# Optimization experiments

Hardware: AMD Instinct MI355X
Metric: run time of the kernel (lower is better)

Reference implementation:

```python
import jax, jax.numpy as jnp
import numpy as np
import math

E = 1024   # embedding_size
H = 16     # layer_size (num heads)
DK = 64    # key_size
DH = 64    # head_size
HID = 4096 # hidden_size
B = 2
S = 2048   # context_size
EPS = 1e-5


def layer_norm(x, w, b):
    mu = jnp.mean(x, axis=-1, keepdims=True)
    var = jnp.mean(jnp.square(x - mu), axis=-1, keepdims=True)
    return (x - mu) * jax.lax.rsqrt(var + EPS) * w + b


def setup_inputs() -> dict:
    key = jax.random.key(0)
    ks = jax.random.split(key, 16)
    sE = 1.0 / math.sqrt(E)
    sH = 1.0 / math.sqrt(HID)
    return {
        "embeddings": jax.random.normal(ks[0], (B, S, E), dtype=jnp.float32),
        "Wq": jax.random.uniform(ks[1], (H, E, DK), minval=-sE, maxval=sE, dtype=jnp.float32),
        "bq": jnp.zeros((H, DK), dtype=jnp.float32),
        "Wk": jax.random.uniform(ks[2], (H, E, DK), minval=-sE, maxval=sE, dtype=jnp.float32),
        "bk": jnp.zeros((H, DK), dtype=jnp.float32),
        "Wv": jax.random.uniform(ks[3], (H, E, DH), minval=-sE, maxval=sE, dtype=jnp.float32),
        "bv": jnp.zeros((H, DH), dtype=jnp.float32),
        "ln1_w": jnp.ones((E,), dtype=jnp.float32),
        "ln1_b": jnp.zeros((E,), dtype=jnp.float32),
        "ln2_w": jnp.ones((E,), dtype=jnp.float32),
        "ln2_b": jnp.zeros((E,), dtype=jnp.float32),
        "W1": jax.random.uniform(ks[4], (E, HID), minval=-sE, maxval=sE, dtype=jnp.float32),
        "b1": jnp.zeros((HID,), dtype=jnp.float32),
        "W2": jax.random.uniform(ks[5], (HID, E), minval=-sH, maxval=sH, dtype=jnp.float32),
        "b2": jnp.zeros((E,), dtype=jnp.float32),
    }


def reference(embeddings, Wq, bq, Wk, bk, Wv, bv, ln1_w, ln1_b, ln2_w, ln2_b, W1, b1, W2, b2):
    # NOTE: faithful to source: residual uses the POST-norm activations
    # (embeddings is reassigned to the LayerNorm output before the residual add).
    x = layer_norm(embeddings, ln1_w, ln1_b)            # [B,S,E]
    q = jnp.einsum('bse,hed->bhsd', x, Wq) + bq[:, None, :]
    k = jnp.einsum('bse,hed->bhsd', x, Wk) + bk[:, None, :]
    v = jnp.einsum('bse,hed->bhsd', x, Wv) + bv[:, None, :]
    scores = jnp.einsum('bhsd,bhtd->bhst', q, k) / math.sqrt(DK)  # [B,H,S,S]
    causal = jnp.tril(jnp.ones((S, S), dtype=bool))
    scores = jnp.where(causal, scores, -jnp.inf)
    w = jax.nn.softmax(scores, axis=-1)
    o = jnp.einsum('bhst,bhtd->bhsd', w, v)             # [B,H,S,DH]
    o = jnp.transpose(o, (0, 2, 1, 3)).reshape(B, S, H * DH)  # concat heads
    x = x + o
    y = layer_norm(x, ln2_w, ln2_b)
    h = jax.nn.relu(jnp.einsum('bse,eh->bsh', y, W1) + b1)
    out = y + jnp.einsum('bsh,he->bse', h, W2) + b2
    return out
```

## Files before the change

kernel.cpp:

```cpp
#include <hip/hip_runtime.h>


typedef unsigned short u16;
typedef unsigned int   u32;
typedef __bf16 bf16x8 __attribute__((ext_vector_type(8)));
typedef float  f32x4  __attribute__((ext_vector_type(4)));

#define NEG_INF (-__builtin_inff())

#if __has_builtin(__builtin_amdgcn_exp2f)
#define EXP2F(x) __builtin_amdgcn_exp2f(x)
#else
#define EXP2F(x) exp2f(x)
#endif

__device__ __forceinline__ u32 pack_bf16_trunc(float a, float b) {
#if __has_builtin(__builtin_amdgcn_perm)
  return __builtin_amdgcn_perm(__float_as_uint(b), __float_as_uint(a), 0x07060302u);
#else
  return (__float_as_uint(a) >> 16) | (__float_as_uint(b) & 0xFFFF0000u);
#endif
}

__device__ __forceinline__ u16 f2b(float f) {
  u32 u = __float_as_uint(f);
  u = (u + 0x7fffu + ((u >> 16) & 1u)) >> 16;
  return (u16)u;
}

__device__ __forceinline__ void gload16(const void* g, void* l) {
  __builtin_amdgcn_global_load_lds(
      (const __attribute__((address_space(1))) u32*)g,
      (__attribute__((address_space(3))) u32*)l, 16, 0, 0);
}

__device__ __forceinline__ bf16x8 ld16(const u16* p) { return *(const bf16x8*)p; }

__device__ __forceinline__
void ln_body(int row, const float* __restrict__ in, const float* __restrict__ in2,
             const float* __restrict__ w, const float* __restrict__ b,
             float* __restrict__ outf, u16* __restrict__ outb) {
  int t = threadIdx.x;
  const float4* ip = (const float4*)(in + (size_t)row * 1024);
  float4 x = ip[t];
  if (in2) {
    const float4* ip2 = (const float4*)(in2 + (size_t)row * 1024);
    float4 o = ip2[t];
    x.x += o.x; x.y += o.y; x.z += o.z; x.w += o.w;
  }
  float s = x.x + x.y + x.z + x.w;
  float q = x.x * x.x + x.y * x.y + x.z * x.z + x.w * x.w;
#pragma unroll
  for (int m = 32; m; m >>= 1) { s += __shfl_xor(s, m); q += __shfl_xor(q, m); }
  __shared__ float rs[4], rq[4];
  if ((t & 63) == 0) { rs[t >> 6] = s; rq[t >> 6] = q; }
  __syncthreads();
  s = rs[0] + rs[1] + rs[2] + rs[3];
  q = rq[0] + rq[1] + rq[2] + rq[3];
  float mean = s * (1.f / 1024.f);
  float var  = q * (1.f / 1024.f) - mean * mean;
  float rstd = rsqrtf(var + 1e-5f);
  float4 wv = ((const float4*)w)[t];
  float4 bv = ((const float4*)b)[t];
  float4 y;
  y.x = (x.x - mean) * rstd * wv.x + bv.x;
  y.y = (x.y - mean) * rstd * wv.y + bv.y;
  y.z = (x.z - mean) * rstd * wv.z + bv.z;
  y.w = (x.w - mean) * rstd * wv.w + bv.w;
  if (outf) ((float4*)(outf + (size_t)row * 1024))[t] = y;
  ushort4 ub;
  ub.x = f2b(y.x); ub.y = f2b(y.y); ub.z = f2b(y.z); ub.w = f2b(y.w);
  ((ushort4*)(outb + (size_t)row * 1024))[t] = ub;
}

__device__ __forceinline__
void trans_body(float* tile, const float* __restrict__ in, u16* __restrict__ out,
                int R, int C, int r0, int c0) {
  int tr = threadIdx.x >> 6, tc = threadIdx.x & 63;
#pragma unroll
  for (int i = 0; i < 16; i++) {
    int r = i * 4 + tr;
    tile[r * 65 + tc] = in[(size_t)(r0 + r) * C + c0 + tc];
  }
  __syncthreads();
#pragma unroll
  for (int i = 0; i < 16; i++) {
    int c = i * 4 + tr;
    out[(size_t)(c0 + c) * R + r0 + tc] = f2b(tile[tc * 65 + c]);
  }
}

__global__ __launch_bounds__(256)
void prologue_k(const float* __restrict__ emb, const float* __restrict__ ln1w,
                const float* __restrict__ ln1b, float* __restrict__ x,
                u16* __restrict__ xb, const float* __restrict__ Wq,
                const float* __restrict__ Wk, const float* __restrict__ Wv,
                u16* __restrict__ Wqkv_t) {
  __shared__ float tile[64 * 65];
  int bx = blockIdx.x;
  if (bx < 4096) {
    ln_body(bx, emb, nullptr, ln1w, ln1b, x, xb);
  } else {
    int id = bx - 4096;
    int z = id >> 4, sub = z & 15, which = z >> 4;
    const float* in = which == 0 ? Wq : (which == 1 ? Wk : Wv);
    trans_body(tile, in + (size_t)sub * 1024 * 64,
               Wqkv_t + (size_t)which * 1024 * 1024 + (size_t)sub * 64 * 1024,
               1024, 64, (id & 15) * 64, 0);
  }
}

__global__ __launch_bounds__(256)
void vtrans_k(const u16* __restrict__ vin, u16* __restrict__ vt) {
  __shared__ __align__(16) u16 tile[64][72];
  int s0 = blockIdx.x * 64, bh = blockIdx.y;
  const u16* ip = vin + (size_t)bh * 2048 * 64;
  u16* op = vt + (size_t)bh * 64 * 2048;
  int t = threadIdx.x;
#pragma unroll
  for (int i = 0; i < 2; i++) {
    int idx = i * 256 + t, r = idx >> 3, c = idx & 7;
    *(uint4*)&tile[r][c * 8] = *(const uint4*)(ip + (size_t)(s0 + r) * 64 + c * 8);
  }
  __syncthreads();
#pragma unroll
  for (int i = 0; i < 16; i++) {
    int d = i * 4 + (t >> 6), s = t & 63;
    op[(size_t)d * 2048 + s0 + s] = tile[s][d];
  }
}

__global__ __launch_bounds__(256)
void ln_k(const float* __restrict__ in, const float* __restrict__ in2,
          const float* __restrict__ w, const float* __restrict__ b,
          float* __restrict__ outf, u16* __restrict__ outb) {
  ln_body(blockIdx.x, in, in2, w, b, outf, outb);
}

#define EPI_QKV  0
#define EPI_RELU 1
#define EPI_RES  2

#define QSCALE 0.18033688011112042f

template <int EPI>
__device__ __forceinline__
void gemm_body(u16* __restrict__ As, u16* __restrict__ Bs,
               const u16* __restrict__ A, const u16* __restrict__ Bt,
               int bxm, int bxn, int kbeg, int klen, int lda, int ldbt,
               const float* __restrict__ bias0, const float* __restrict__ bias1,
               const float* __restrict__ bias2, const float* __restrict__ res,
               int ldout, u16* __restrict__ outb, float* __restrict__ outf,
               float* __restrict__ p1, float* __restrict__ p2, int z) {
  int t = threadIdx.x;
  int wave = t >> 6, lane = t & 63, quad = lane >> 4, l16 = lane & 15;
  int x7 = l16 & 7;
  int wm = (wave >> 1) * 64, wn = (wave & 1) * 64;
  int bm = bxm * 128, bn = bxn * 128;

  const u16* Agl[4];
  const u16* Bgl[4];
#pragma unroll
  for (int i = 0; i < 4; i++) {
    int idx = i * 256 + t, r = idx >> 3, c = (idx & 7) ^ (r & 7);
    Agl[i] = A + (size_t)(bm + r) * lda + kbeg + c * 8;
    Bgl[i] = Bt + (size_t)(bn + r) * ldbt + kbeg + c * 8;
  }
  u16* Asl = As + t * 8;
  u16* Bsl = Bs + t * 8;

  f32x4 acc[4][4] = {};

  for (int k0 = 0; k0 < klen; k0 += 64) {
#pragma unroll
    for (int i = 0; i < 4; i++) {
      gload16(Agl[i] + k0, Asl + i * 2048);
      gload16(Bgl[i] + k0, Bsl + i * 2048);
    }
    __syncthreads();
#pragma unroll
    for (int kc = 0; kc < 2; kc++) {
      bf16x8 af[4], bfr[4];
#pragma unroll
      for (int i = 0; i < 4; i++) {
        int r = wm + i * 16 + l16;
        af[i] = *(const bf16x8*)(As + r * 64 + (((kc * 4 + quad) ^ x7) * 8));
      }
#pragma unroll
      for (int j = 0; j < 4; j++) {
        int r = wn + j * 16 + l16;
        bfr[j] = *(const bf16x8*)(Bs + r * 64 + (((kc * 4 + quad) ^ x7) * 8));
      }
#pragma unroll
      for (int i = 0; i < 4; i++)
#pragma unroll
        for (int j = 0; j < 4; j++)
          acc[i][j] = __builtin_amdgcn_mfma_f32_16x16x32_bf16(af[i], bfr[j],
                                                              acc[i][j], 0, 0, 0);
    }
    __syncthreads();
  }

#pragma unroll
  for (int i = 0; i < 4; i++) {
#pragma unroll
    for (int j = 0; j < 4; j++) {
      int c = bn + wn + j * 16 + l16;
#pragma unroll
      for (int rr = 0; rr < 4; rr++) {
        int r = bm + wm + i * 16 + quad * 4 + rr;
        float v = acc[i][j][rr];
        if (EPI == EPI_QKV) {
          int which = c >> 10, h = (c >> 6) & 15, d = c & 63;
          const float* bp = which == 0 ? bias0 : (which == 1 ? bias1 : bias2);
          v += bp[h * 64 + d];
          if (which == 0) v *= QSCALE;
          int bb = r >> 11, ss = r & 2047;
          outb[((size_t)(which * 32 + bb * 16 + h) * 2048 + ss) * 64 + d] = f2b(v);
        } else if (EPI == EPI_RELU) {
          v += bias0[c];
          v = v > 0.f ? v : 0.f;
          outb[(size_t)r * ldout + c] = f2b(v);
        } else {
          if (z == 0) {
            v += bias0[c] + res[(size_t)r * ldout + c];
            outf[(size_t)r * ldout + c] = v;
          } else if (z == 1) {
            p1[(size_t)r * ldout + c] = v;
          } else {
            p2[(size_t)r * ldout + c] = v;
          }
        }
      }
    }
  }
}

__global__ __launch_bounds__(256)
void qkv_plus_k(const u16* __restrict__ xb, const u16* __restrict__ Wqkv_t,
                const float* __restrict__ bq, const float* __restrict__ bk,
                const float* __restrict__ bv, u16* __restrict__ qkvb,
                const float* __restrict__ W1, const float* __restrict__ W2,
                u16* __restrict__ W1t, u16* __restrict__ W2t) {
  __shared__ __align__(16) u16 SM[2][128 * 64];
  int bx = blockIdx.x;
  if (bx < 768) {
    gemm_body<EPI_QKV>(SM[0], SM[1], xb, Wqkv_t, bx & 31, bx >> 5, 0, 1024,
                       1024, 1024, bq, bk, bv, nullptr, 0, qkvb, nullptr,
                       nullptr, nullptr, 0);
  } else {
    int id = bx - 768;
    float* tile = (float*)SM;
    if (id < 1024)
      trans_body(tile, W1, W1t, 1024, 4096, (id & 15) * 64, (id >> 4) * 64);
    else {
      id -= 1024;
      trans_body(tile, W2, W2t, 4096, 1024, (id >> 4) * 64, (id & 15) * 64);
    }
  }
}

__global__ __launch_bounds__(256)
void ffn1_gemm(const u16* __restrict__ A, const u16* __restrict__ Bt,
               const float* __restrict__ b0, u16* __restrict__ outb) {
  __shared__ __align__(16) u16 SM[2][128 * 64];
  gemm_body<EPI_RELU>(SM[0], SM[1], A, Bt, blockIdx.x, blockIdx.y, 0, 1024,
                      1024, 1024, b0, nullptr, nullptr, nullptr, 4096, outb,
                      nullptr, nullptr, nullptr, 0);
}

__global__ __launch_bounds__(256)
void ffn2_gemm(const u16* __restrict__ A, const u16* __restrict__ Bt,
               const float* __restrict__ b0, const float* __restrict__ res,
               float* __restrict__ outf, float* __restrict__ p1,
               float* __restrict__ p2) {
  __shared__ __align__(16) u16 SM[2][128 * 64];
  int z = blockIdx.z;
  int kbeg = z * 1344 + (z > 0 ? 64 : 0);
  int klen = 1344 + (z == 0 ? 64 : 0);
  gemm_body<EPI_RES>(SM[0], SM[1], A, Bt, blockIdx.x, blockIdx.y, kbeg, klen,
                     4096, 4096, b0, nullptr, nullptr, res, 1024, nullptr,
                     outf, p1, p2, z);
}

__global__ __launch_bounds__(256)
void reduce2_k(float* __restrict__ out, const float* __restrict__ p1,
               const float* __restrict__ p2) {
  int i = blockIdx.x * 256 + threadIdx.x;
  float4 a = ((const float4*)p1)[i];
  float4 c = ((const float4*)p2)[i];
  float4 b = ((float4*)out)[i];
  b.x += a.x + c.x; b.y += a.y + c.y; b.z += a.z + c.z; b.w += a.w + c.w;
  ((float4*)out)[i] = b;
}

__global__ __launch_bounds__(512, 6)
void attn_k(const u16* __restrict__ qkv, const u16* __restrict__ vt,
            float* __restrict__ o) {
  int bh = blockIdx.y, b = bh >> 4, h = bh & 15;
  int Qt = b ? (15 - (int)blockIdx.x) : (int)blockIdx.x;
  int t = threadIdx.x;
  int wave = t >> 6, lane = t & 63, quad = lane >> 4, l16 = lane & 15;
  int x7 = l16 & 7;
  int q0 = Qt * 128 + wave * 16;

  const u16* qg = qkv + (size_t)bh * (2048 * 64);
  const u16* kg = qkv + (size_t)(32 + bh) * (2048 * 64);
  const u16* vg = vt + (size_t)bh * (64 * 2048);

  __shared__ __align__(16) u16 Ks[2][64 * 64];
  __shared__ __align__(16) u16 Vs[2][64 * 64];
  __shared__ __align__(16) u16 Ps[8][16 * 64 + 32];
  u16* Pw = Ps[wave];
  float* auxf = (float*)(Pw + 1024);

  int sr = t >> 3, sc_ = (t & 7) ^ (sr & 7);

  gload16(kg + (size_t)sr * 64 + sc_ * 8, Ks[0] + t * 8);
  gload16(vg + (size_t)sr * 2048 + sc_ * 8, Vs[0] + t * 8);

  bf16x8 qf0 = ld16(qg + (size_t)(q0 + l16) * 64 + quad * 8);
  bf16x8 qf1 = ld16(qg + (size_t)(q0 + l16) * 64 + 32 + quad * 8);

  f32x4 oacc[4] = {};
  float mo = NEG_INF, ll = 0.f;
  int kmax_w = q0 >> 6;
  int klast = 2 * Qt + 1;

  __syncthreads();

  for (int kt = 0; kt <= klast; kt++) {
    const u16* ks = Ks[kt & 1];
    const u16* vs = Vs[kt & 1];
    if (kt < klast) {
      gload16(kg + (size_t)((kt + 1) * 64 + sr) * 64 + sc_ * 8, Ks[(kt + 1) & 1] + t * 8);
      gload16(vg + (size_t)sr * 2048 + (kt + 1) * 64 + sc_ * 8, Vs[(kt + 1) & 1] + t * 8);
    }
    if (kt <= kmax_w) {
      f32x4 sc[4];
#pragma unroll
      for (int g = 0; g < 4; g++) {
        const u16* kr = ks + (g * 16 + l16) * 64;
        bf16x8 kf0 = *(const bf16x8*)(kr + ((quad ^ x7) * 8));
        bf16x8 kf1 = *(const bf16x8*)(kr + (((4 + quad) ^ x7) * 8));
        f32x4 s = {};
        s = __builtin_amdgcn_mfma_f32_16x16x32_bf16(kf0, qf0, s, 0, 0, 0);
        s = __builtin_amdgcn_mfma_f32_16x16x32_bf16(kf1, qf1, s, 0, 0, 0);
        sc[g] = s;
      }

      if (kt == kmax_w) {
#pragma unroll
        for (int g = 0; g < 4; g++) {
          int kvb = kt * 64 + g * 16 + quad * 4;
#pragma unroll
          for (int rr = 0; rr < 4; rr++)
            if (kvb + rr > q0 + l16) sc[g][rr] = NEG_INF;
        }
      }

      float mx = sc[0][0];
#pragma unroll
      for (int g = 0; g < 4; g++)
#pragma unroll
        for (int rr = 0; rr < 4; rr++) mx = fmaxf(mx, sc[g][rr]);
      mx = fmaxf(mx, __shfl_xor(mx, 16));
      mx = fmaxf(mx, __shfl_xor(mx, 32));
      float mnew = fmaxf(mo, mx);
      float al = EXP2F(mo - mnew);
      mo = mnew;

      float sum = 0.f;
#pragma unroll
      for (int g = 0; g < 4; g++) {
        float p0 = EXP2F(sc[g][0] - mnew);
        float p1 = EXP2F(sc[g][1] - mnew);
        float p2 = EXP2F(sc[g][2] - mnew);
        float p3 = EXP2F(sc[g][3] - mnew);
        sum += (p0 + p1) + (p2 + p3);
        u32 lo = pack_bf16_trunc(p0, p1);
        u32 hi = pack_bf16_trunc(p2, p3);
        int slot = (2 * g + (quad >> 1)) ^ x7;
        *(uint2*)(Pw + l16 * 64 + slot * 8 + (quad & 1) * 4) = make_uint2(lo, hi);
      }
      sum += __shfl_xor(sum, 16);
      sum += __shfl_xor(sum, 32);
      ll = ll * al + sum;

      if (lane < 16) auxf[lane] = al;
      f32x4 av = *(const f32x4*)(auxf + quad * 4);
#pragma unroll
      for (int g = 0; g < 4; g++)
#pragma unroll
        for (int rr = 0; rr < 4; rr++) oacc[g][rr] *= av[rr];

      bf16x8 pf0 = *(const bf16x8*)(Pw + l16 * 64 + ((quad ^ x7) * 8));
      bf16x8 pf1 = *(const bf16x8*)(Pw + l16 * 64 + (((4 + quad) ^ x7) * 8));
#pragma unroll
      for (int g = 0; g < 4; g++) {
        const u16* vr = vs + (g * 16 + l16) * 64;
        bf16x8 vf0 = *(const bf16x8*)(vr + ((quad ^ x7) * 8));
        bf16x8 vf1 = *(const bf16x8*)(vr + (((4 + quad) ^ x7) * 8));
        oacc[g] = __builtin_amdgcn_mfma_f32_16x16x32_bf16(pf0, vf0, oacc[g], 0, 0, 0);
        oacc[g] = __builtin_amdgcn_mfma_f32_16x16x32_bf16(pf1, vf1, oacc[g], 0, 0, 0);
      }
    }
    __syncthreads();
  }

  if (lane < 16) auxf[lane] = ll;
  f32x4 lv = *(const f32x4*)(auxf + quad * 4);
  float rinv[4];
#pragma unroll
  for (int rr = 0; rr < 4; rr++) rinv[rr] = 1.f / lv[rr];
  float* op = o + ((size_t)b * 2048 + q0) * 1024 + h * 64;
#pragma unroll
  for (int g = 0; g < 4; g++)
#pragma unroll
    for (int rr = 0; rr < 4; rr++)
      op[(size_t)(quad * 4 + rr) * 1024 + g * 16 + l16] = oacc[g][rr] * rinv[rr];
}

extern "C" void kernel_launch(void* const* d_in, const int* in_sizes, int n_in,
                              void* d_out, int out_size, void* d_ws, size_t ws_size,
                              hipStream_t stream) {
  const float* emb  = (const float*)d_in[0];
  const float* Wq   = (const float*)d_in[1];
  const float* bq   = (const float*)d_in[2];
  const float* Wk   = (const float*)d_in[3];
  const float* bk   = (const float*)d_in[4];
  const float* Wv   = (const float*)d_in[5];
  const float* bv   = (const float*)d_in[6];
  const float* ln1w = (const float*)d_in[7];
  const float* ln1b = (const float*)d_in[8];
  const float* ln2w = (const float*)d_in[9];
  const float* ln2b = (const float*)d_in[10];
  const float* W1   = (const float*)d_in[11];
  const float* b1   = (const float*)d_in[12];
  const float* W2   = (const float*)d_in[13];
  const float* b2   = (const float*)d_in[14];
  float* out = (float*)d_out;

  char* p = (char*)d_ws;
  u16*   Wqkv_t = (u16*)p;   p += (size_t)3072 * 1024 * 2;
  u16*   W2t    = (u16*)p;   p += (size_t)1024 * 4096 * 2;
  u16*   W1t    = (u16*)p;   p += (size_t)4096 * 1024 * 2;
  float* x      = (float*)p; p += (size_t)4096 * 1024 * 4;
  u16*   xb     = (u16*)p;   p += (size_t)4096 * 1024 * 2;
  u16*   qkvb   = (u16*)p;   p += (size_t)3 * 32 * 2048 * 64 * 2;
  float* ob     = (float*)p; p += (size_t)4096 * 1024 * 4;
  float* y      = (float*)p; p += (size_t)4096 * 1024 * 4;
  u16*   yb     = (u16*)p;   p += (size_t)4096 * 1024 * 2;
  u16*   hb     = (u16*)qkvb;
  u16*   vT     = (u16*)y;
  float* part1  = (float*)W1t;
  float* part2  = (float*)((char*)x + (size_t)4096 * 1024 * 2);
  if (ws_size < (size_t)(p - (char*)d_ws)) return;

  prologue_k<<<dim3(4096 + 768), 256, 0, stream>>>(
      emb, ln1w, ln1b, x, xb, Wq, Wk, Wv, Wqkv_t);

  qkv_plus_k<<<dim3(768 + 2048), 256, 0, stream>>>(
      xb, Wqkv_t, bq, bk, bv, qkvb, W1, W2, W1t, W2t);

  vtrans_k<<<dim3(32, 32), 256, 0, stream>>>(qkvb + (size_t)64 * 2048 * 64, vT);

  attn_k<<<dim3(16, 32), 512, 0, stream>>>(qkvb, vT, ob);

  ln_k<<<dim3(4096), 256, 0, stream>>>(x, ob, ln2w, ln2b, y, yb);

  ffn1_gemm<<<dim3(32, 32), 256, 0, stream>>>(yb, W1t, b1, hb);

  ffn2_gemm<<<dim3(32, 8, 3), 256, 0, stream>>>(hb, W2t, b2, y, out, part1, part2);

  reduce2_k<<<dim3(4096), 256, 0, stream>>>(out, part1, part2);
}
```

Measured before the change: 336.0 us.

## Have each attention wave own two query tiles and cut FFN2 split-K to two

The attention kernel now runs 4 waves of 256 threads instead of 8 waves of 512. Each wave handles two 16-row query groups 64 rows apart, so the K and V fragments read from shared memory are loaded once per tile and reused for both groups. This cuts LDS traffic but raises register pressure, and the launch bounds change to 3 blocks per CU. Separately, the FFN2 split-K drops from three slices to two, which removes one partial buffer and lightens the reduction, at the cost of fewer blocks and longer K loops per block.

```diff
diff --git a/kernel.cpp b/kernel.cpp
--- a/kernel.cpp
+++ b/kernel.cpp
@@ -151,7 +151,7 @@
                const float* __restrict__ bias0, const float* __restrict__ bias1,
                const float* __restrict__ bias2, const float* __restrict__ res,
                int ldout, u16* __restrict__ outb, float* __restrict__ outf,
-               float* __restrict__ p1, float* __restrict__ p2, int z) {
+               float* __restrict__ p1, int z) {
   int t = threadIdx.x;
   int wave = t >> 6, lane = t & 63, quad = lane >> 4, l16 = lane & 15;
   int x7 = l16 & 7;
@@ -225,10 +225,8 @@
           if (z == 0) {
             v += bias0[c] + res[(size_t)r * ldout + c];
             outf[(size_t)r * ldout + c] = v;
-          } else if (z == 1) {
+          } else {
             p1[(size_t)r * ldout + c] = v;
-          } else {
-            p2[(size_t)r * ldout + c] = v;
           }
         }
       }
@@ -247,7 +245,7 @@
   if (bx < 768) {
     gemm_body<EPI_QKV>(SM[0], SM[1], xb, Wqkv_t, bx & 31, bx >> 5, 0, 1024,
                        1024, 1024, bq, bk, bv, nullptr, 0, qkvb, nullptr,
-                       nullptr, nullptr, 0);
+                       nullptr, 0);
   } else {
     int id = bx - 768;
     float* tile = (float*)SM;
@@ -266,35 +264,30 @@
   __shared__ __align__(16) u16 SM[2][128 * 64];
   gemm_body<EPI_RELU>(SM[0], SM[1], A, Bt, blockIdx.x, blockIdx.y, 0, 1024,
                       1024, 1024, b0, nullptr, nullptr, nullptr, 4096, outb,
-                      nullptr, nullptr, nullptr, 0);
+                      nullptr, nullptr, 0);
 }
 
 __global__ __launch_bounds__(256)
 void ffn2_gemm(const u16* __restrict__ A, const u16* __restrict__ Bt,
                const float* __restrict__ b0, const float* __restrict__ res,
-               float* __restrict__ outf, float* __restrict__ p1,
-               float* __restrict__ p2) {
+               float* __restrict__ outf, float* __restrict__ p1) {
   __shared__ __align__(16) u16 SM[2][128 * 64];
   int z = blockIdx.z;
-  int kbeg = z * 1344 + (z > 0 ? 64 : 0);
-  int klen = 1344 + (z == 0 ? 64 : 0);
-  gemm_body<EPI_RES>(SM[0], SM[1], A, Bt, blockIdx.x, blockIdx.y, kbeg, klen,
+  gemm_body<EPI_RES>(SM[0], SM[1], A, Bt, blockIdx.x, blockIdx.y, z * 2048, 2048,
                      4096, 4096, b0, nullptr, nullptr, res, 1024, nullptr,
-                     outf, p1, p2, z);
-}
-
-__global__ __launch_bounds__(256)
-void reduce2_k(float* __restrict__ out, const float* __restrict__ p1,
-               const float* __restrict__ p2) {
+                     outf, p1, z);
+}
+
+__global__ __launch_bounds__(256)
+void reduce_k(float* __restrict__ out, const float* __restrict__ p1) {
   int i = blockIdx.x * 256 + threadIdx.x;
   float4 a = ((const float4*)p1)[i];
-  float4 c = ((const float4*)p2)[i];
   float4 b = ((float4*)out)[i];
-  b.x += a.x + c.x; b.y += a.y + c.y; b.z += a.z + c.z; b.w += a.w + c.w;
+  b.x += a.x; b.y += a.y; b.z += a.z; b.w += a.w;
   ((float4*)out)[i] = b;
 }
 
-__global__ __launch_bounds__(512, 6)
+__global__ __launch_bounds__(256, 3)
 void attn_k(const u16* __restrict__ qkv, const u16* __restrict__ vt,
             float* __restrict__ o) {
   int bh = blockIdx.y, b = bh >> 4, h = bh & 15;
@@ -302,7 +295,7 @@
   int t = threadIdx.x;
   int wave = t >> 6, lane = t & 63, quad = lane >> 4, l16 = lane & 15;
   int x7 = l16 & 7;
-  int q0 = Qt * 128 + wave * 16;
+  int qb = Qt * 128 + wave * 16;
 
   const u16* qg = qkv + (size_t)bh * (2048 * 64);
   const u16* kg = qkv + (size_t)(32 + bh) * (2048 * 64);
@@ -311,20 +304,24 @@
   __shared__ __align__(16) u16 Ks[2][64 * 64];
   __shared__ __align__(16) u16 Vs[2][64 * 64];
   __shared__ __align__(16) u16 Ps[8][16 * 64 + 32];
-  u16* Pw = Ps[wave];
-  float* auxf = (float*)(Pw + 1024);
-
-  int sr = t >> 3, sc_ = (t & 7) ^ (sr & 7);
-
-  gload16(kg + (size_t)sr * 64 + sc_ * 8, Ks[0] + t * 8);
-  gload16(vg + (size_t)sr * 2048 + sc_ * 8, Vs[0] + t * 8);
-
-  bf16x8 qf0 = ld16(qg + (size_t)(q0 + l16) * 64 + quad * 8);
-  bf16x8 qf1 = ld16(qg + (size_t)(q0 + l16) * 64 + 32 + quad * 8);
-
-  f32x4 oacc[4] = {};
-  float mo = NEG_INF, ll = 0.f;
-  int kmax_w = q0 >> 6;
+
+#pragma unroll
+  for (int i = 0; i < 2; i++) {
+    int idx = i * 256 + t, r = idx >> 3, c = (idx & 7) ^ (r & 7);
+    gload16(kg + (size_t)r * 64 + c * 8, Ks[0] + idx * 8);
+    gload16(vg + (size_t)r * 2048 + c * 8, Vs[0] + idx * 8);
+  }
+
+  bf16x8 qf[2][2];
+#pragma unroll
+  for (int G = 0; G < 2; G++) {
+    const u16* qr = qg + (size_t)(qb + G * 64 + l16) * 64;
+    qf[G][0] = ld16(qr + quad * 8);
+    qf[G][1] = ld16(qr + 32 + quad * 8);
+  }
+
+  f32x4 oacc[2][4] = {};
+  float mo[2] = {NEG_INF, NEG_INF}, ll[2] = {0.f, 0.f};
   int klast = 2 * Qt + 1;
 
   __syncthreads();
@@ -333,23 +330,42 @@
     const u16* ks = Ks[kt & 1];
     const u16* vs = Vs[kt & 1];
     if (kt < klast) {
-      gload16(kg + (size_t)((kt + 1) * 64 + sr) * 64 + sc_ * 8, Ks[(kt + 1) & 1] + t * 8);
-      gload16(vg + (size_t)sr * 2048 + (kt + 1) * 64 + sc_ * 8, Vs[(kt + 1) & 1] + t * 8);
-    }
-    if (kt <= kmax_w) {
+#pragma unroll
+      for (int i = 0; i < 2; i++) {
+        int idx = i * 256 + t, r = idx >> 3, c = (idx & 7) ^ (r & 7);
+        gload16(kg + (size_t)((kt + 1) * 64 + r) * 64 + c * 8, Ks[(kt + 1) & 1] + idx * 8);
+        gload16(vg + (size_t)r * 2048 + (kt + 1) * 64 + c * 8, Vs[(kt + 1) & 1] + idx * 8);
+      }
+    }
+
+    bf16x8 kf[4][2], vf[4][2];
+#pragma unroll
+    for (int g = 0; g < 4; g++) {
+      const u16* kr = ks + (g * 16 + l16) * 64;
+      kf[g][0] = *(const bf16x8*)(kr + ((quad ^ x7) * 8));
+      kf[g][1] = *(const bf16x8*)(kr + (((4 + quad) ^ x7) * 8));
+      const u16* vr = vs + (g * 16 + l16) * 64;
+      vf[g][0] = *(const bf16x8*)(vr + ((quad ^ x7) * 8));
+      vf[g][1] = *(const bf16x8*)(vr + (((4 + quad) ^ x7) * 8));
+    }
+
+#pragma unroll
+    for (int G = 0; G < 2; G++) {
+      int kdiag = klast - 1 + G;
+      if (kt > kdiag) continue;
+      int q0 = qb + G * 64;
+      u16* Pw = Ps[wave * 2 + G];
+      float* auxf = (float*)(Pw + 1024);
+
       f32x4 sc[4];
 #pragma unroll
       for (int g = 0; g < 4; g++) {
-        const u16* kr = ks + (g * 16 + l16) * 64;
-        bf16x8 kf0 = *(const bf16x8*)(kr + ((quad ^ x7) * 8));
-        bf16x8 kf1 = *(const bf16x8*)(kr + (((4 + quad) ^ x7) * 8));
         f32x4 s = {};
-        s = __builtin_amdgcn_mfma_f32_16x16x32_bf16(kf0, qf0, s, 0, 0, 0);
-        s = __builtin_amdgcn_mfma_f32_16x16x32_bf16(kf1, qf1, s, 0, 0, 0);
+        s = __builtin_amdgcn_mfma_f32_16x16x32_bf16(kf[g][0], qf[G][0], s, 0, 0, 0);
+        s = __builtin_amdgcn_mfma_f32_16x16x32_bf16(kf[g][1], qf[G][1], s, 0, 0, 0);
         sc[g] = s;
       }
-
-      if (kt == kmax_w) {
+      if (kt == kdiag) {
 #pragma unroll
         for (int g = 0; g < 4; g++) {
           int kvb = kt * 64 + g * 16 + quad * 4;
@@ -366,9 +382,9 @@
         for (int rr = 0; rr < 4; rr++) mx = fmaxf(mx, sc[g][rr]);
       mx = fmaxf(mx, __shfl_xor(mx, 16));
       mx = fmaxf(mx, __shfl_xor(mx, 32));
-      float mnew = fmaxf(mo, mx);
-      float al = EXP2F(mo - mnew);
-      mo = mnew;
+      float mnew = fmaxf(mo[G], mx);
+      float al = EXP2F(mo[G] - mnew);
+      mo[G] = mnew;
 
       float sum = 0.f;
 #pragma unroll
@@ -385,40 +401,42 @@
       }
       sum += __shfl_xor(sum, 16);
       sum += __shfl_xor(sum, 32);
-      ll = ll * al + sum;
+      ll[G] = ll[G] * al + sum;
 
       if (lane < 16) auxf[lane] = al;
       f32x4 av = *(const f32x4*)(auxf + quad * 4);
 #pragma unroll
       for (int g = 0; g < 4; g++)
 #pragma unroll
-        for (int rr = 0; rr < 4; rr++) oacc[g][rr] *= av[rr];
+        for (int rr = 0; rr < 4; rr++) oacc[G][g][rr] *= av[rr];
 
       bf16x8 pf0 = *(const bf16x8*)(Pw + l16 * 64 + ((quad ^ x7) * 8));
       bf16x8 pf1 = *(const bf16x8*)(Pw + l16 * 64 + (((4 + quad) ^ x7) * 8));
 #pragma unroll
       for (int g = 0; g < 4; g++) {
-        const u16* vr = vs + (g * 16 + l16) * 64;
-        bf16x8 vf0 = *(const bf16x8*)(vr + ((quad ^ x7) * 8));
-        bf16x8 vf1 = *(const bf16x8*)(vr + (((4 + quad) ^ x7) * 8));
-        oacc[g] = __builtin_amdgcn_mfma_f32_16x16x32_bf16(pf0, vf0, oacc[g], 0, 0, 0);
-        oacc[g] = __builtin_amdgcn_mfma_f32_16x16x32_bf16(pf1, vf1, oacc[g], 0, 0, 0);
+        oacc[G][g] = __builtin_amdgcn_mfma_f32_16x16x32_bf16(pf0, vf[g][0], oacc[G][g], 0, 0, 0);
+        oacc[G][g] = __builtin_amdgcn_mfma_f32_16x16x32_bf16(pf1, vf[g][1], oacc[G][g], 0, 0, 0);
       }
     }
     __syncthreads();
   }
 
-  if (lane < 16) auxf[lane] = ll;
-  f32x4 lv = *(const f32x4*)(auxf + quad * 4);
-  float rinv[4];
-#pragma unroll
-  for (int rr = 0; rr < 4; rr++) rinv[rr] = 1.f / lv[rr];
-  float* op = o + ((size_t)b * 2048 + q0) * 1024 + h * 64;
-#pragma unroll
-  for (int g = 0; g < 4; g++)
-#pragma unroll
-    for (int rr = 0; rr < 4; rr++)
-      op[(size_t)(quad * 4 + rr) * 1024 + g * 16 + l16] = oacc[g][rr] * rinv[rr];
+#pragma unroll
+  for (int G = 0; G < 2; G++) {
+    u16* Pw = Ps[wave * 2 + G];
+    float* auxf = (float*)(Pw + 1024);
+    if (lane < 16) auxf[lane] = ll[G];
+    f32x4 lv = *(const f32x4*)(auxf + quad * 4);
+    float rinv[4];
+#pragma unroll
+    for (int rr = 0; rr < 4; rr++) rinv[rr] = 1.f / lv[rr];
+    float* op = o + ((size_t)b * 2048 + qb + G * 64) * 1024 + h * 64;
+#pragma unroll
+    for (int g = 0; g < 4; g++)
+#pragma unroll
+      for (int rr = 0; rr < 4; rr++)
+        op[(size_t)(quad * 4 + rr) * 1024 + g * 16 + l16] = oacc[G][g][rr] * rinv[rr];
+  }
 }
 
 extern "C" void kernel_launch(void* const* d_in, const int* in_sizes, int n_in,
@@ -454,7 +472,6 @@
   u16*   hb     = (u16*)qkvb;
   u16*   vT     = (u16*)y;
   float* part1  = (float*)W1t;
-  float* part2  = (float*)((char*)x + (size_t)4096 * 1024 * 2);
   if (ws_size < (size_t)(p - (char*)d_ws)) return;
 
   prologue_k<<<dim3(4096 + 768), 256, 0, stream>>>(
@@ -465,13 +482,13 @@
 
   vtrans_k<<<dim3(32, 32), 256, 0, stream>>>(qkvb + (size_t)64 * 2048 * 64, vT);
 
-  attn_k<<<dim3(16, 32), 512, 0, stream>>>(qkvb, vT, ob);
+  attn_k<<<dim3(16, 32), 256, 0, stream>>>(qkvb, vT, ob);
 
   ln_k<<<dim3(4096), 256, 0, stream>>>(x, ob, ln2w, ln2b, y, yb);
 
   ffn1_gemm<<<dim3(32, 32), 256, 0, stream>>>(yb, W1t, b1, hb);
 
-  ffn2_gemm<<<dim3(32, 8, 3), 256, 0, stream>>>(hb, W2t, b2, y, out, part1, part2);
-
-  reduce2_k<<<dim3(4096), 256, 0, stream>>>(out, part1, part2);
-}
+  ffn2_gemm<<<dim3(32, 8, 2), 256, 0, stream>>>(hb, W2t, b2, y, out, part1);
+
+  reduce_k<<<dim3(4096), 256, 0, stream>>>(out, part1);
+}
```

Result: no change. 338.0 us (+0.6%).
